# Kernel optimization log

Hardware: AMD Instinct MI355X
Metric: run time of the kernel (lower is better)

The kernel has to match this reference:

```python
import jax, jax.numpy as jnp
import numpy as np

NUM_USR = 8192
H = 256  # NUM_SOURCE == H (feature dim of y_a); NUM_TARGET = 256


def setup_inputs() -> dict:
    key = jax.random.key(0)
    k1, k2, k3, k4 = jax.random.split(key, 4)
    return {
        "y_a": jax.random.normal(k1, (NUM_USR, H), dtype=jnp.float32),
        "y_b": jax.random.normal(k2, (NUM_USR, H), dtype=jnp.float32),
        "W": jax.random.normal(k3, (H, H), dtype=jnp.float32) * (1.0 / np.sqrt(H)),
        "b": jax.random.normal(k4, (H,), dtype=jnp.float32) * 0.01,
    }


def reference(y_a, y_b, W, b):
    # Linear: proj[j] = W @ y_b[j] + b   (torch nn.Linear convention)
    proj = jnp.einsum("jt,st->js", y_b, W) + b          # [num_usr, H]
    # torch loop computes score[i, j] = y_a[i] . proj[j], replicated H times
    # then averaged: out[i, k] = (1/H) * sum_j sigmoid(score[i, j])
    scores = jnp.einsum("ih,jh->ij", y_a, proj)          # [num_usr, num_usr]
    s = jnp.sum(jax.nn.sigmoid(scores), axis=1) / y_a.shape[1]  # [num_usr]
    return jnp.broadcast_to(s[:, None], y_a.shape)       # [num_usr, H]
```

## Files before the change

### kernel.cpp

```cpp
#include <hip/hip_runtime.h>

#define NUSR 8192
#define HDIM 256

typedef __attribute__((ext_vector_type(8))) __bf16 bf16x8;
typedef __attribute__((ext_vector_type(4))) float f32x4;

union frag_u { bf16x8 v; unsigned short u[8]; };

__device__ __forceinline__ unsigned short f2bf(float f) {
  unsigned u = __builtin_bit_cast(unsigned, f);
  u += 0x7FFFu + ((u >> 16) & 1u);
  return (unsigned short)(u >> 16);
}

__device__ __forceinline__ float sigmoidf_fast(float x) {
  float e = __builtin_amdgcn_exp2f(x * -1.44269504088896340736f);
  return __builtin_amdgcn_rcpf(1.0f + e);
}

__global__ __launch_bounds__(256) void k1_proj(
    const float* __restrict__ ya, const float* __restrict__ yb,
    const float* __restrict__ W, const float* __restrict__ bvec,
    unsigned short* __restrict__ Zbf, unsigned short* __restrict__ ybf,
    float* __restrict__ cvec)
{
  __shared__ __align__(16) unsigned short wt[64 * 264];
  const int tid  = threadIdx.x;
  const int lane = tid & 63;
  const int w    = tid >> 6;
  const int quad = lane >> 4;
  const int l15  = lane & 15;
  const int bx = blockIdx.x;
  const int by = blockIdx.y;
  const int bid = by * 64 + bx;

  {
    const float4* src = (const float4*)yb + (size_t)bid * 2048;
    unsigned short* dst = ybf + (size_t)bid * 8192;
#pragma unroll
    for (int i = 0; i < 8; ++i) {
      float4 v = src[i * 256 + tid];
      ushort4 o;
      o.x = f2bf(v.x); o.y = f2bf(v.y); o.z = f2bf(v.z); o.w = f2bf(v.w);
      *(ushort4*)(dst + (size_t)(i * 256 + tid) * 4) = o;
    }
  }

  for (int p = 0; p < 64; ++p) {
    int lin = p * 256 + tid;
    int s = lin >> 6;
    int tc = lin & 63;
    wt[tc * 264 + s] = f2bf(W[s * 256 + by * 64 + tc]);
  }
  __syncthreads();

  const int rbase = bx * 128 + w * 32;

  frag_u A[2][8];
  float cpart[2] = {0.f, 0.f};
#pragma unroll
  for (int h = 0; h < 2; ++h) {
    const float* yarow = ya + (size_t)(rbase + h * 16 + l15) * HDIM;
#pragma unroll
    for (int kb = 0; kb < 8; ++kb) {
      const int k0 = kb * 32 + quad * 8;
      float vv[8];
#pragma unroll
      for (int j = 0; j < 8; ++j) vv[j] = yarow[k0 + j];
#pragma unroll
      for (int j = 0; j < 8; ++j) A[h][kb].u[j] = f2bf(vv[j]);
#pragma unroll
      for (int j = 0; j < 8; ++j) cpart[h] += vv[j] * bvec[k0 + j];
    }
  }
#pragma unroll
  for (int off = 16; off < 64; off <<= 1) {
    cpart[0] += __shfl_xor(cpart[0], off, 64);
    cpart[1] += __shfl_xor(cpart[1], off, 64);
  }
  if (by == 0 && lane < 16) {
    cvec[rbase + lane]      = cpart[0];
    cvec[rbase + 16 + lane] = cpart[1];
  }

#pragma unroll
  for (int tt = 0; tt < 4; ++tt) {
    f32x4 a0 = {0.f,0.f,0.f,0.f}, a1 = {0.f,0.f,0.f,0.f};
#pragma unroll
    for (int kb = 0; kb < 8; ++kb) {
      bf16x8 bfrag = *(const bf16x8*)&wt[(tt * 16 + l15) * 264 + kb * 32 + quad * 8];
      a0 = __builtin_amdgcn_mfma_f32_16x16x32_bf16(A[0][kb].v, bfrag, a0, 0, 0, 0);
      a1 = __builtin_amdgcn_mfma_f32_16x16x32_bf16(A[1][kb].v, bfrag, a1, 0, 0, 0);
    }
    const int col = by * 64 + tt * 16 + l15;
#pragma unroll
    for (int r = 0; r < 4; ++r) {
      Zbf[(size_t)(rbase + quad * 4 + r) * HDIM + col]      = f2bf(a0[r]);
      Zbf[(size_t)(rbase + 16 + quad * 4 + r) * HDIM + col] = f2bf(a1[r]);
    }
  }
}

__global__ __launch_bounds__(256) void k2_score(
    const unsigned short* __restrict__ Zbf, const unsigned short* __restrict__ ybf,
    const float* __restrict__ cvec, float* __restrict__ svec)
{
  __shared__ __align__(16) unsigned short bs[64 * 264];
  const int tid  = threadIdx.x;
  const int lane = tid & 63;
  const int w    = tid >> 6;
  const int quad = lane >> 4;
  const int l15  = lane & 15;
  const int rbase = blockIdx.x * 128 + w * 32;
  const int cbase = blockIdx.y * 1024;

  frag_u A[2][8];
#pragma unroll
  for (int h = 0; h < 2; ++h)
#pragma unroll
    for (int kb = 0; kb < 8; ++kb)
      A[h][kb].v = *(const bf16x8*)&Zbf[(size_t)(rbase + h * 16 + l15) * HDIM + kb * 32 + quad * 8];

  float crow[2][4];
#pragma unroll
  for (int h = 0; h < 2; ++h)
#pragma unroll
    for (int r = 0; r < 4; ++r)
      crow[h][r] = cvec[rbase + h * 16 + quad * 4 + r];

  float rs[2][4] = {{0.f,0.f,0.f,0.f},{0.f,0.f,0.f,0.f}};

  for (int st = 0; st < 16; ++st) {
    __syncthreads();
    {
      const uint4* src = (const uint4*)(ybf + (size_t)(cbase + st * 64) * HDIM);
#pragma unroll
      for (int p = 0; p < 8; ++p) {
        int lin = p * 256 + tid;
        int row = lin >> 5, ch = lin & 31;
        *(uint4*)&bs[row * 264 + ch * 8] = src[row * 32 + ch];
      }
    }
    __syncthreads();
#pragma unroll
    for (int tt = 0; tt < 4; ++tt) {
      f32x4 a0 = {0.f,0.f,0.f,0.f}, a1 = {0.f,0.f,0.f,0.f};
#pragma unroll
      for (int kb = 0; kb < 8; ++kb) {
        bf16x8 bfrag = *(const bf16x8*)&bs[(tt * 16 + l15) * 264 + kb * 32 + quad * 8];
        a0 = __builtin_amdgcn_mfma_f32_16x16x32_bf16(A[0][kb].v, bfrag, a0, 0, 0, 0);
        a1 = __builtin_amdgcn_mfma_f32_16x16x32_bf16(A[1][kb].v, bfrag, a1, 0, 0, 0);
      }
#pragma unroll
      for (int r = 0; r < 4; ++r) {
        rs[0][r] += sigmoidf_fast(a0[r] + crow[0][r]);
        rs[1][r] += sigmoidf_fast(a1[r] + crow[1][r]);
      }
    }
  }

#pragma unroll
  for (int off = 1; off < 16; off <<= 1) {
#pragma unroll
    for (int h = 0; h < 2; ++h)
#pragma unroll
      for (int r = 0; r < 4; ++r)
        rs[h][r] += __shfl_xor(rs[h][r], off, 64);
  }
  if (l15 == 0) {
#pragma unroll
    for (int h = 0; h < 2; ++h)
#pragma unroll
      for (int r = 0; r < 4; ++r)
        atomicAdd(&svec[rbase + h * 16 + quad * 4 + r], rs[h][r]);
  }
}

__global__ __launch_bounds__(256) void k3_bcast(
    const float* __restrict__ svec, float* __restrict__ out)
{
  int idx = blockIdx.x * 256 + threadIdx.x;
  int row = idx >> 6;
  float v = svec[row] * (1.0f / 256.0f);
  float4 o = {v, v, v, v};
  ((float4*)out)[idx] = o;
}

extern "C" void kernel_launch(void* const* d_in, const int* in_sizes, int n_in,
                              void* d_out, int out_size, void* d_ws, size_t ws_size,
                              hipStream_t stream) {
  (void)in_sizes; (void)n_in; (void)out_size;
  const float* ya = (const float*)d_in[0];
  const float* yb = (const float*)d_in[1];
  const float* W  = (const float*)d_in[2];
  const float* bv = (const float*)d_in[3];
  float* out = (float*)d_out;

  char* ws = (char*)d_ws;
  unsigned short *Zbf, *ybf;
  float *cvec, *svec;
  const size_t need = (8ull << 20) + (64ull << 10);
  if (ws_size >= need) {
    Zbf  = (unsigned short*)ws;
    ybf  = (unsigned short*)(ws + (4 << 20));
    cvec = (float*)(ws + (8 << 20));
    svec = (float*)(ws + (8 << 20) + (32 << 10));
  } else {
    Zbf  = (unsigned short*)d_out;
    ybf  = (unsigned short*)((char*)d_out + (4 << 20));
    cvec = (float*)ws;
    svec = (float*)(ws + (32 << 10));
  }

  hipMemsetAsync(svec, 0, NUSR * sizeof(float), stream);
  k1_proj<<<dim3(64, 4), 256, 0, stream>>>(ya, yb, W, bv, Zbf, ybf, cvec);
  k2_score<<<dim3(64, 8), 256, 0, stream>>>(Zbf, ybf, cvec, svec);
  k3_bcast<<<2048, 256, 0, stream>>>(svec, out);
}
```

Before: 127.2 us.

## Project y_b directly with bias and convert y_a to bf16 inside score kernel

Instead of computing Z = y_a·W plus a per-row bias-dot vector and a separate bf16 copy of y_b, the projection kernel now computes proj = y_b·Wᵀ + b directly in bf16. The score kernel reads y_a in fp32 and converts it to bf16 fragments itself, so the cvec term and the ybf staging buffer go away. The score grid is doubled to 64x16 with half the columns per block to raise occupancy. The projection kernel loads W straight from global memory per lane with no LDS transpose, and each score block re-reads and re-converts y_a, which adds redundant global traffic.

```diff
diff --git a/kernel.cpp b/kernel.cpp
--- a/kernel.cpp
+++ b/kernel.cpp
@@ -20,91 +20,60 @@
 }
 
 __global__ __launch_bounds__(256) void k1_proj(
-    const float* __restrict__ ya, const float* __restrict__ yb,
-    const float* __restrict__ W, const float* __restrict__ bvec,
-    unsigned short* __restrict__ Zbf, unsigned short* __restrict__ ybf,
-    float* __restrict__ cvec)
+    const float* __restrict__ yb, const float* __restrict__ W,
+    const float* __restrict__ bvec, unsigned short* __restrict__ Pbf)
 {
-  __shared__ __align__(16) unsigned short wt[64 * 264];
   const int tid  = threadIdx.x;
   const int lane = tid & 63;
   const int w    = tid >> 6;
   const int quad = lane >> 4;
   const int l15  = lane & 15;
-  const int bx = blockIdx.x;
-  const int by = blockIdx.y;
-  const int bid = by * 64 + bx;
-
-  {
-    const float4* src = (const float4*)yb + (size_t)bid * 2048;
-    unsigned short* dst = ybf + (size_t)bid * 8192;
-#pragma unroll
-    for (int i = 0; i < 8; ++i) {
-      float4 v = src[i * 256 + tid];
-      ushort4 o;
-      o.x = f2bf(v.x); o.y = f2bf(v.y); o.z = f2bf(v.z); o.w = f2bf(v.w);
-      *(ushort4*)(dst + (size_t)(i * 256 + tid) * 4) = o;
-    }
-  }
-
-  for (int p = 0; p < 64; ++p) {
-    int lin = p * 256 + tid;
-    int s = lin >> 6;
-    int tc = lin & 63;
-    wt[tc * 264 + s] = f2bf(W[s * 256 + by * 64 + tc]);
-  }
-  __syncthreads();
-
-  const int rbase = bx * 128 + w * 32;
+  const int rb   = blockIdx.x * 32;
 
   frag_u A[2][8];
-  float cpart[2] = {0.f, 0.f};
 #pragma unroll
   for (int h = 0; h < 2; ++h) {
-    const float* yarow = ya + (size_t)(rbase + h * 16 + l15) * HDIM;
+    const float* src = yb + (size_t)(rb + h * 16 + l15) * HDIM;
 #pragma unroll
     for (int kb = 0; kb < 8; ++kb) {
-      const int k0 = kb * 32 + quad * 8;
-      float vv[8];
-#pragma unroll
-      for (int j = 0; j < 8; ++j) vv[j] = yarow[k0 + j];
-#pragma unroll
-      for (int j = 0; j < 8; ++j) A[h][kb].u[j] = f2bf(vv[j]);
-#pragma unroll
-      for (int j = 0; j < 8; ++j) cpart[h] += vv[j] * bvec[k0 + j];
+      float4 v0 = *(const float4*)&src[kb * 32 + quad * 8];
+      float4 v1 = *(const float4*)&src[kb * 32 + quad * 8 + 4];
+      A[h][kb].u[0] = f2bf(v0.x); A[h][kb].u[1] = f2bf(v0.y);
+      A[h][kb].u[2] = f2bf(v0.z); A[h][kb].u[3] = f2bf(v0.w);
+      A[h][kb].u[4] = f2bf(v1.x); A[h][kb].u[5] = f2bf(v1.y);
+      A[h][kb].u[6] = f2bf(v1.z); A[h][kb].u[7] = f2bf(v1.w);
     }
-  }
-#pragma unroll
-  for (int off = 16; off < 64; off <<= 1) {
-    cpart[0] += __shfl_xor(cpart[0], off, 64);
-    cpart[1] += __shfl_xor(cpart[1], off, 64);
-  }
-  if (by == 0 && lane < 16) {
-    cvec[rbase + lane]      = cpart[0];
-    cvec[rbase + 16 + lane] = cpart[1];
   }
 
 #pragma unroll
   for (int tt = 0; tt < 4; ++tt) {
+    const int scol = w * 64 + tt * 16 + l15;
+    const float* wrow = W + (size_t)scol * HDIM;
     f32x4 a0 = {0.f,0.f,0.f,0.f}, a1 = {0.f,0.f,0.f,0.f};
 #pragma unroll
     for (int kb = 0; kb < 8; ++kb) {
-      bf16x8 bfrag = *(const bf16x8*)&wt[(tt * 16 + l15) * 264 + kb * 32 + quad * 8];
-      a0 = __builtin_amdgcn_mfma_f32_16x16x32_bf16(A[0][kb].v, bfrag, a0, 0, 0, 0);
-      a1 = __builtin_amdgcn_mfma_f32_16x16x32_bf16(A[1][kb].v, bfrag, a1, 0, 0, 0);
+      float4 v0 = *(const float4*)&wrow[kb * 32 + quad * 8];
+      float4 v1 = *(const float4*)&wrow[kb * 32 + quad * 8 + 4];
+      frag_u B;
+      B.u[0] = f2bf(v0.x); B.u[1] = f2bf(v0.y);
+      B.u[2] = f2bf(v0.z); B.u[3] = f2bf(v0.w);
+      B.u[4] = f2bf(v1.x); B.u[5] = f2bf(v1.y);
+      B.u[6] = f2bf(v1.z); B.u[7] = f2bf(v1.w);
+      a0 = __builtin_amdgcn_mfma_f32_16x16x32_bf16(A[0][kb].v, B.v, a0, 0, 0, 0);
+      a1 = __builtin_amdgcn_mfma_f32_16x16x32_bf16(A[1][kb].v, B.v, a1, 0, 0, 0);
     }
-    const int col = by * 64 + tt * 16 + l15;
+    const float bcol = bvec[scol];
 #pragma unroll
     for (int r = 0; r < 4; ++r) {
-      Zbf[(size_t)(rbase + quad * 4 + r) * HDIM + col]      = f2bf(a0[r]);
-      Zbf[(size_t)(rbase + 16 + quad * 4 + r) * HDIM + col] = f2bf(a1[r]);
+      Pbf[(size_t)(rb + quad * 4 + r) * HDIM + scol]      = f2bf(a0[r] + bcol);
+      Pbf[(size_t)(rb + 16 + quad * 4 + r) * HDIM + scol] = f2bf(a1[r] + bcol);
     }
   }
 }
 
 __global__ __launch_bounds__(256) void k2_score(
-    const unsigned short* __restrict__ Zbf, const unsigned short* __restrict__ ybf,
-    const float* __restrict__ cvec, float* __restrict__ svec)
+    const float* __restrict__ ya, const unsigned short* __restrict__ Pbf,
+    float* __restrict__ svec)
 {
   __shared__ __align__(16) unsigned short bs[64 * 264];
   const int tid  = threadIdx.x;
@@ -113,28 +82,29 @@
   const int quad = lane >> 4;
   const int l15  = lane & 15;
   const int rbase = blockIdx.x * 128 + w * 32;
-  const int cbase = blockIdx.y * 1024;
+  const int cbase = blockIdx.y * 512;
 
   frag_u A[2][8];
 #pragma unroll
-  for (int h = 0; h < 2; ++h)
+  for (int h = 0; h < 2; ++h) {
+    const float* src = ya + (size_t)(rbase + h * 16 + l15) * HDIM;
 #pragma unroll
-    for (int kb = 0; kb < 8; ++kb)
-      A[h][kb].v = *(const bf16x8*)&Zbf[(size_t)(rbase + h * 16 + l15) * HDIM + kb * 32 + quad * 8];
-
-  float crow[2][4];
-#pragma unroll
-  for (int h = 0; h < 2; ++h)
-#pragma unroll
-    for (int r = 0; r < 4; ++r)
-      crow[h][r] = cvec[rbase + h * 16 + quad * 4 + r];
+    for (int kb = 0; kb < 8; ++kb) {
+      float4 v0 = *(const float4*)&src[kb * 32 + quad * 8];
+      float4 v1 = *(const float4*)&src[kb * 32 + quad * 8 + 4];
+      A[h][kb].u[0] = f2bf(v0.x); A[h][kb].u[1] = f2bf(v0.y);
+      A[h][kb].u[2] = f2bf(v0.z); A[h][kb].u[3] = f2bf(v0.w);
+      A[h][kb].u[4] = f2bf(v1.x); A[h][kb].u[5] = f2bf(v1.y);
+      A[h][kb].u[6] = f2bf(v1.z); A[h][kb].u[7] = f2bf(v1.w);
+    }
+  }
 
   float rs[2][4] = {{0.f,0.f,0.f,0.f},{0.f,0.f,0.f,0.f}};
 
-  for (int st = 0; st < 16; ++st) {
+  for (int st = 0; st < 8; ++st) {
     __syncthreads();
     {
-      const uint4* src = (const uint4*)(ybf + (size_t)(cbase + st * 64) * HDIM);
+      const uint4* src = (const uint4*)(Pbf + (size_t)(cbase + st * 64) * HDIM);
 #pragma unroll
       for (int p = 0; p < 8; ++p) {
         int lin = p * 256 + tid;
@@ -154,8 +124,8 @@
       }
 #pragma unroll
       for (int r = 0; r < 4; ++r) {
-        rs[0][r] += sigmoidf_fast(a0[r] + crow[0][r]);
-        rs[1][r] += sigmoidf_fast(a1[r] + crow[1][r]);
+        rs[0][r] += sigmoidf_fast(a0[r]);
+        rs[1][r] += sigmoidf_fast(a1[r]);
       }
     }
   }
@@ -198,23 +168,19 @@
   float* out = (float*)d_out;
 
   char* ws = (char*)d_ws;
-  unsigned short *Zbf, *ybf;
-  float *cvec, *svec;
-  const size_t need = (8ull << 20) + (64ull << 10);
+  unsigned short* Pbf;
+  float* svec;
+  const size_t need = (4ull << 20) + (32ull << 10);
   if (ws_size >= need) {
-    Zbf  = (unsigned short*)ws;
-    ybf  = (unsigned short*)(ws + (4 << 20));
-    cvec = (float*)(ws + (8 << 20));
-    svec = (float*)(ws + (8 << 20) + (32 << 10));
+    Pbf  = (unsigned short*)ws;
+    svec = (float*)(ws + (4 << 20));
   } else {
-    Zbf  = (unsigned short*)d_out;
-    ybf  = (unsigned short*)((char*)d_out + (4 << 20));
-    cvec = (float*)ws;
-    svec = (float*)(ws + (32 << 10));
+    Pbf  = (unsigned short*)d_out;
+    svec = (float*)ws;
   }
 
   hipMemsetAsync(svec, 0, NUSR * sizeof(float), stream);
-  k1_proj<<<dim3(64, 4), 256, 0, stream>>>(ya, yb, W, bv, Zbf, ybf, cvec);
-  k2_score<<<dim3(64, 8), 256, 0, stream>>>(Zbf, ybf, cvec, svec);
+  k1_proj<<<256, 256, 0, stream>>>(yb, W, bv, Pbf);
+  k2_score<<<dim3(64, 16), 256, 0, stream>>>(ya, Pbf, svec);
   k3_bcast<<<2048, 256, 0, stream>>>(svec, out);
 }
```

Measured after the change: 131.8 us. 1.04x slower.
